# Kernel tuning notes

Measured on AMD Instinct MI355X. Metric: run time of the kernel, lower is better.

## Reference

```python
import jax, jax.numpy as jnp
import numpy as np

H, D, J, T, IN = 8, 32, 22, 6, 256   # heads, head_dim, joint_num, time_len-2, input_dim
S = 3 * J                            # sequence axis of attention (66)
NEG = -9e15


def _domain_mask():
    m = np.ones((S, S), np.float32)
    m[0:J, 2 * J:3 * J] = 0.0
    m[2 * J:3 * J, 0:J] = 0.0
    return jnp.asarray(m)


def setup_inputs() -> dict:
    key = jax.random.key(0)
    ks = jax.random.split(key, 5)
    s = 0.02
    return {
        "x": jax.random.normal(ks[0], (512, T, S, IN), jnp.float32),
        "Wq": jax.random.normal(ks[1], (H * D, IN), jnp.float32) * s,
        "bq": jnp.zeros((H * D,), jnp.float32),
        "Wk": jax.random.normal(ks[2], (H * D, IN), jnp.float32) * s,
        "bk": jnp.zeros((H * D,), jnp.float32),
        "Wv": jax.random.normal(ks[3], (H * D, IN), jnp.float32) * s,
        "bv": jnp.zeros((H * D,), jnp.float32),
        "Wc": jax.random.normal(ks[4], (J, S), jnp.float32) * s,
        "bc": jnp.zeros((J,), jnp.float32),
    }


def reference(x, Wq, bq, Wk, bk, Wv, bv, Wc, bc):
    B = x.shape[0]
    mask = _domain_mask()

    def proj(W, b):
        # (B,T,S,IN) @ (IN,H*D) -> (B,T,S,H,D) -> (B,T,H,S,D)
        return (x @ W.T + b).reshape(B, T, S, H, D).transpose(0, 1, 3, 2, 4)

    q = proj(Wq, bq)
    k = proj(Wk, bk)
    v = jax.nn.relu(proj(Wv, bv))

    scores = jnp.einsum('bthqd,bthkd->bthqk', q, k) / jnp.sqrt(jnp.float32(D))
    scores = scores * mask
    # joint_num == 22 branch: threshold-based pruning against row max
    m = jnp.max(scores, axis=-1, keepdims=True)
    scores = jnp.where(jnp.abs(scores) <= m / 9.0, NEG, scores)
    attn = jax.nn.softmax(scores, axis=-1)

    out = jnp.einsum('bthqk,bthkd->bthqd', attn, v)          # (B,T,H,S,D)
    # cls Linear over the S axis: (B,T,H,D,S) -> (B,T,H,D,J), then back to (B,T,H,J,D)
    out = jnp.einsum('bthsd,js->bthjd', out, Wc) + bc[None, None, None, :, None]
    out = out.transpose(0, 1, 3, 2, 4)                        # (B,T,J,H,D)
    return out.reshape(B, T * J, H * D)
```

## Files before the change

### kernel.cpp

```cpp
#include <hip/hip_runtime.h>
#include <hip/hip_bf16.h>


constexpr int T  = 6;
constexpr int S  = 66;
constexpr int IN = 256;
constexpr int H  = 8;
constexpr int D  = 32;
constexpr int J  = 22;
constexpr float NEG = -9e15f;
constexpr float INV_SQRT_D = 0.17677669529663688110f;

#define XH_OFF   0
#define XL_OFF   9216
#define WH_OFF   18432
#define WL_OFF   30720
#define QH_OFF   0
#define QL_OFF   4752
#define KH_OFF   9504
#define KL_OFF   14256
#define SC_OFF   19008
#define VTH_OFF  36432
#define VTL_OFF  43088
#define INV_OFF  49744
#define PH_OFF   0
#define PL_OFF   13728
#define AOT_OFF  27456
#define WCH_OFF  36432
#define WCL_OFF  43088
#define SMEM_BYTES 50008

#define WSW_STRIDE 24576
#define WSWC_OFF   786432
#define WS_W       799744ull
#define XIMG_OFF   799744
#define XIMG_BT    73728
#define WS_FULL    (799744ull + 3072ull * 73728ull)

typedef float f32x4  __attribute__((ext_vector_type(4)));
typedef short bf16x8 __attribute__((ext_vector_type(8)));
typedef short s4v    __attribute__((ext_vector_type(4)));

__device__ __forceinline__ unsigned cvtpk(float a, float b) {
    unsigned r;
    asm("v_cvt_pk_bf16_f32 %0, %1, %2" : "=v"(r) : "v"(a), "v"(b));
    return r;
}
__device__ __forceinline__ float bfh2f(unsigned short h) {
    return __uint_as_float(((unsigned)h) << 16);
}
__device__ __forceinline__ void split2(float a, float b, unsigned& hi, unsigned& lo) {
    unsigned h = cvtpk(a, b);
    float ra = a - __uint_as_float(h << 16);
    float rb = b - __uint_as_float(h & 0xffff0000u);
    lo = cvtpk(ra, rb);
    hi = h;
}
__device__ __forceinline__ bf16x8 ld_bf16x8_a8(const short* p) {
    s4v a = *(const s4v*)p;
    s4v b = *(const s4v*)(p + 4);
    return __builtin_shufflevector(a, b, 0, 1, 2, 3, 4, 5, 6, 7);
}
__device__ __forceinline__ void gload16(const void* g, void* l) {
    __builtin_amdgcn_global_load_lds(
        (const __attribute__((address_space(1))) unsigned*)g,
        (__attribute__((address_space(3))) unsigned*)l, 16, 0, 0);
}

__global__ __launch_bounds__(256)
void presplit_kernel(const float* __restrict__ Wq, const float* __restrict__ Wk,
                     const float* __restrict__ Wv, const float* __restrict__ Wc,
                     unsigned char* __restrict__ ws)
{
    int gid = blockIdx.x * 256 + threadIdx.x;
    if (gid < 49152) {
        int c   = gid & 15;
        int r2  = gid >> 4;
        int row = r2 % 96;
        int r3  = r2 / 96;
        int mat = row >> 5, dd = row & 31;
        int chunk = r3 & 3, hh = r3 >> 2;
        const float* Wm = (mat == 0) ? Wq : (mat == 1) ? Wk : Wv;
        float4 v = *(const float4*)(Wm + (size_t)(hh * 32 + dd) * IN + chunk * 64 + c * 4);
        uint2 hi, lo;
        split2(v.x, v.y, hi.x, lo.x);
        split2(v.z, v.w, hi.y, lo.y);
        unsigned base = (unsigned)r3 * WSW_STRIDE;
        unsigned rel  = (unsigned)(((row << 7) + (c << 3)) ^ ((row & 7) << 4));
        *(uint2*)(ws + base + rel)         = hi;
        *(uint2*)(ws + base + 12288 + rel) = lo;
    } else if (gid < 49152 + 1664) {
        int g2  = gid - 49152;
        int row = g2 / 52, cu = g2 - row * 52;
        int c0  = 2 * cu;
        float a = (row < 22 && c0     < 66) ? Wc[row * 66 + c0]     : 0.f;
        float b = (row < 22 && c0 + 1 < 66) ? Wc[row * 66 + c0 + 1] : 0.f;
        unsigned hi, lo;
        split2(a, b, hi, lo);
        *(unsigned*)(ws + WSWC_OFF + row * 208 + 4 * cu)        = hi;
        *(unsigned*)(ws + WSWC_OFF + 6656 + row * 208 + 4 * cu) = lo;
    }
}

__global__ __launch_bounds__(256)
void presplit_x_kernel(const float* __restrict__ x, unsigned char* __restrict__ ws)
{
    int gid = blockIdx.x * 256 + threadIdx.x;
    if (gid >= 3072 * 66 * 64) return;
    int c16  = gid & 63;
    int rest = gid >> 6;
    int s  = rest % 66;
    int bt = rest / 66;
    int chunk = c16 >> 4, c = c16 & 15;
    float4 v = *(const float4*)(x + (size_t)(bt * 66 + s) * 256 + c16 * 4);
    uint2 hi, lo;
    split2(v.x, v.y, hi.x, lo.x);
    split2(v.z, v.w, hi.y, lo.y);
    unsigned rel = (unsigned)(((s << 7) + (c << 3)) ^ ((s & 7) << 4));
    unsigned char* img = ws + XIMG_OFF + (size_t)bt * XIMG_BT + chunk * 18432;
    *(uint2*)(img + rel)        = hi;
    *(uint2*)(img + 9216 + rel) = lo;
}

template<int MODE>
__global__ __launch_bounds__(256, 3)
void mha_fused_kernel(const float* __restrict__ x,
                      const float* __restrict__ Wq, const float* __restrict__ bq,
                      const float* __restrict__ Wk, const float* __restrict__ bk,
                      const float* __restrict__ Wv, const float* __restrict__ bv,
                      const float* __restrict__ Wc, const float* __restrict__ bc,
                      const unsigned char* __restrict__ ws,
                      float* __restrict__ out)
{
    __shared__ __align__(16) unsigned char smem[SMEM_BYTES];

    const int tid = threadIdx.x;
    const int i0  = blockIdx.x;
    const int h   = (i0 >> 3) & 7;
    const int bt  = (i0 & 7) | ((i0 >> 6) << 3);

    const int wid  = tid >> 6;
    const int lane = tid & 63;
    const int l15  = lane & 15;
    const int quad = lane >> 4;
    const int swz  = (l15 & 7) << 4;

    f32x4 accs[8];
    #pragma unroll
    for (int jj = 0; jj < 8; ++jj) accs[jj] = (f32x4){0.f, 0.f, 0.f, 0.f};

    for (int chunk = 0; chunk < 4; ++chunk) {
        __syncthreads();
        if constexpr (MODE == 2) {
            const unsigned char* ximg = ws + XIMG_OFF + (size_t)bt * XIMG_BT + chunk * 18432;
            const unsigned char* wimg = ws + (unsigned)((h << 2) | chunk) * WSW_STRIDE;
            for (int i = wid; i < 18; i += 4)
                gload16(ximg + (i << 10) + (lane << 4), smem + XH_OFF + (i << 10));
            for (int i = wid; i < 24; i += 4)
                gload16(wimg + (i << 10) + (lane << 4), smem + WH_OFF + (i << 10));
        } else {
            if constexpr (MODE == 1) {
                const unsigned char* wimg = ws + (unsigned)((h << 2) | chunk) * WSW_STRIDE;
                for (int i = wid; i < 24; i += 4)
                    gload16(wimg + (i << 10) + (lane << 4), smem + WH_OFF + (i << 10));
            } else {
                for (int u = tid; u < 1536; u += 256) {
                    int row = u >> 4, c = u & 15;
                    int mat = row >> 5, dd = row & 31;
                    const float* Wm = (mat == 0) ? Wq : (mat == 1) ? Wk : Wv;
                    float4 v = *(const float4*)(Wm + (size_t)(h * 32 + dd) * IN + chunk * 64 + c * 4);
                    uint2 hi, lo;
                    split2(v.x, v.y, hi.x, lo.x);
                    split2(v.z, v.w, hi.y, lo.y);
                    int rel = ((row << 7) + (c << 3)) ^ ((row & 7) << 4);
                    *(uint2*)(smem + WH_OFF + rel) = hi;
                    *(uint2*)(smem + WL_OFF + rel) = lo;
                }
            }
            const float* xg = x + (size_t)bt * S * IN + chunk * 64;
            for (int u = tid; u < 1056; u += 256) {
                int s = u >> 4, c = u & 15;
                float4 v = *(const float4*)(xg + (size_t)s * IN + c * 4);
                uint2 hi, lo;
                split2(v.x, v.y, hi.x, lo.x);
                split2(v.z, v.w, hi.y, lo.y);
                int rel = ((s << 7) + (c << 3)) ^ ((s & 7) << 4);
                *(uint2*)(smem + XH_OFF + rel) = hi;
                *(uint2*)(smem + XL_OFF + rel) = lo;
            }
        }
        __syncthreads();

        const unsigned char* sb = smem;
        for (int jj = 0; jj < 8; ++jj) {
            int j = wid + 4 * jj;
            if (j >= 30) break;
            int mat = j / 10, rr = j - mat * 10;
            int mtile = rr >> 1, ntile = rr & 1;
            int abase = XH_OFF + ((mtile * 16 + l15) << 7);
            int bbase = WH_OFF + (((mat << 5) + (ntile << 4) + l15) << 7);
            #pragma unroll
            for (int kk = 0; kk < 2; ++kk) {
                int off = ((quad << 4) + (kk << 6)) ^ swz;
                bf16x8 ah = *(const bf16x8*)(sb + abase + off);
                bf16x8 al = *(const bf16x8*)(sb + abase + 9216 + off);
                bf16x8 bh = *(const bf16x8*)(sb + bbase + off);
                bf16x8 bl = *(const bf16x8*)(sb + bbase + 12288 + off);
                accs[jj] = __builtin_amdgcn_mfma_f32_16x16x32_bf16(ah, bh, accs[jj], 0, 0, 0);
                accs[jj] = __builtin_amdgcn_mfma_f32_16x16x32_bf16(ah, bl, accs[jj], 0, 0, 0);
                accs[jj] = __builtin_amdgcn_mfma_f32_16x16x32_bf16(al, bh, accs[jj], 0, 0, 0);
            }
        }
    }
    __syncthreads();

    {
        short* qh = (short*)(smem + QH_OFF); short* ql = (short*)(smem + QL_OFF);
        short* kh = (short*)(smem + KH_OFF); short* kl = (short*)(smem + KL_OFF);
        for (int jj = 0; jj < 8; ++jj) {
            int j = wid + 4 * jj;
            if (j >= 30) break;
            int mat = j / 10, rr = j - mat * 10;
            int mtile = rr >> 1, ntile = rr & 1;
            int dd = ntile * 16 + l15;
            const float* bias_p = (mat == 0) ? bq : (mat == 1) ? bk : bv;
            float bias = bias_p[h * 32 + dd];
            int sbase = mtile * 16 + quad * 4;
            if (mat < 2) {
                short* bh_ = (mat == 0) ? qh : kh;
                short* bl_ = (mat == 0) ? ql : kl;
                uint2 hi, lo;
                split2(accs[jj][0] + bias, accs[jj][1] + bias, hi.x, lo.x);
                split2(accs[jj][2] + bias, accs[jj][3] + bias, hi.y, lo.y);
                unsigned hs[4] = { hi.x & 0xffffu, hi.x >> 16, hi.y & 0xffffu, hi.y >> 16 };
                unsigned ls[4] = { lo.x & 0xffffu, lo.x >> 16, lo.y & 0xffffu, lo.y >> 16 };
                #pragma unroll
                for (int reg = 0; reg < 4; ++reg) {
                    int s = sbase + reg;
                    if (s < 66) {
                        bh_[s * 36 + dd] = (short)hs[reg];
                        bl_[s * 36 + dd] = (short)ls[reg];
                    }
                }
            } else {
                float vv[4];
                #pragma unroll
                for (int reg = 0; reg < 4; ++reg) {
                    int s = sbase + reg;
                    vv[reg] = (s < 66) ? fmaxf(accs[jj][reg] + bias, 0.f) : 0.f;
                }
                uint2 ph, pl;
                split2(vv[0], vv[1], ph.x, pl.x);
                split2(vv[2], vv[3], ph.y, pl.y);
                *(uint2*)(smem + VTH_OFF + dd * 208 + 2 * sbase) = ph;
                *(uint2*)(smem + VTL_OFF + dd * 208 + 2 * sbase) = pl;
            }
        }
        for (int u = tid; u < 512; u += 256) {
            int comp = u >= 256 ? 1 : 0, rem = comp ? u - 256 : u;
            int row = rem >> 3, kcol = 80 + 2 * (rem & 7);
            *(unsigned*)(smem + (comp ? VTL_OFF : VTH_OFF) + row * 208 + 2 * kcol) = 0u;
        }
    }
    __syncthreads();

    {
        const short* qh = (const short*)(smem + QH_OFF);
        const short* ql = (const short*)(smem + QL_OFF);
        const short* kh = (const short*)(smem + KH_OFF);
        const short* kl = (const short*)(smem + KL_OFF);
        float* sc = (float*)(smem + SC_OFF);
        for (int t = 0; t < 7; ++t) {
            int tt = wid + 4 * t;
            if (tt >= 25) break;
            int mq = tt / 5, mk = tt - mq * 5;
            int aoff = (mq * 16 + l15) * 36 + quad * 8;
            int boff = (mk * 16 + l15) * 36 + quad * 8;
            bf16x8 ah = ld_bf16x8_a8(qh + aoff);
            bf16x8 al = ld_bf16x8_a8(ql + aoff);
            bf16x8 bh = ld_bf16x8_a8(kh + boff);
            bf16x8 bl = ld_bf16x8_a8(kl + boff);
            f32x4 acc = (f32x4){0.f, 0.f, 0.f, 0.f};
            acc = __builtin_amdgcn_mfma_f32_16x16x32_bf16(ah, bh, acc, 0, 0, 0);
            acc = __builtin_amdgcn_mfma_f32_16x16x32_bf16(ah, bl, acc, 0, 0, 0);
            acc = __builtin_amdgcn_mfma_f32_16x16x32_bf16(al, bh, acc, 0, 0, 0);
            int ks = mk * 16 + l15;
            #pragma unroll
            for (int reg = 0; reg < 4; ++reg) {
                int qs = mq * 16 + quad * 4 + reg;
                if (qs < 66 && ks < 66) {
                    bool masked = (qs < J && ks >= 2 * J) || (qs >= 2 * J && ks < J);
                    sc[qs * 66 + ks] = masked ? 0.f : acc[reg] * INV_SQRT_D;
                }
            }
        }
    }
    __syncthreads();

    {
        const float* sc = (const float*)(smem + SC_OFF);
        const int group = tid >> 4, lane16 = tid & 15;
        const int rbase = ((group & 3) << 2) + (group >> 2);
        float val[5][5];
        #pragma unroll
        for (int i = 0; i < 5; ++i) {
            int r = rbase + 16 * i;
            #pragma unroll
            for (int tt = 0; tt < 5; ++tt) {
                int c = lane16 + 16 * tt;
                val[i][tt] = (r < 66 && c < 66) ? sc[r * 66 + c] : -INFINITY;
            }
        }
        __syncthreads();

        short* Ph = (short*)(smem + PH_OFF);
        short* Pl = (short*)(smem + PL_OFF);
        float* inv = (float*)(smem + INV_OFF);
        #pragma unroll
        for (int i = 0; i < 5; ++i) {
            int r = rbase + 16 * i;
            if (r >= 66) continue;
            float m = -INFINITY;
            #pragma unroll
            for (int tt = 0; tt < 5; ++tt) m = fmaxf(m, val[i][tt]);
            m = fmaxf(m, __shfl_xor(m, 1));
            m = fmaxf(m, __shfl_xor(m, 2));
            m = fmaxf(m, __shfl_xor(m, 4));
            m = fmaxf(m, __shfl_xor(m, 8));
            const float thr = m / 9.0f;
            float e[5], lsum = 0.f, rmax = -INFINITY;
            #pragma unroll
            for (int tt = 0; tt < 5; ++tt) {
                float sv = val[i][tt];
                float pr = (fabsf(sv) <= thr) ? NEG : sv;
                val[i][tt] = pr;
                rmax = fmaxf(rmax, pr);
            }
            rmax = fmaxf(rmax, __shfl_xor(rmax, 1));
            rmax = fmaxf(rmax, __shfl_xor(rmax, 2));
            rmax = fmaxf(rmax, __shfl_xor(rmax, 4));
            rmax = fmaxf(rmax, __shfl_xor(rmax, 8));
            #pragma unroll
            for (int tt = 0; tt < 5; ++tt) {
                int c = lane16 + 16 * tt;
                float ev = (c < 66) ? __expf(val[i][tt] - rmax) : 0.f;
                e[tt] = ev;
                lsum += ev;
            }
            lsum += __shfl_xor(lsum, 1);
            lsum += __shfl_xor(lsum, 2);
            lsum += __shfl_xor(lsum, 4);
            lsum += __shfl_xor(lsum, 8);
            #pragma unroll
            for (int tt = 0; tt < 6; ++tt) {
                int c = lane16 + 16 * tt;
                unsigned short hi = 0, lo = 0;
                if (c < 66) {
                    float ev = e[tt];
                    hi = (unsigned short)cvtpk(ev, ev);
                    lo = (unsigned short)cvtpk(ev - bfh2f(hi), 0.f);
                }
                if (c < 96) {
                    Ph[r * 104 + c] = (short)hi;
                    Pl[r * 104 + c] = (short)lo;
                }
            }
            if (lane16 == 0) inv[r] = 1.0f / lsum;
        }
    }
    __syncthreads();

    {
        const short* Ph = (const short*)(smem + PH_OFF);
        const short* Pl = (const short*)(smem + PL_OFF);
        const short* vh = (const short*)(smem + VTH_OFF);
        const short* vl = (const short*)(smem + VTL_OFF);
        const float* inv = (const float*)(smem + INV_OFF);
        for (int t = 0; t < 3; ++t) {
            int tt = wid + 4 * t;
            if (tt >= 10) break;
            int mq = tt >> 1, nd = tt & 1;
            f32x4 acc = (f32x4){0.f, 0.f, 0.f, 0.f};
            #pragma unroll
            for (int ks = 0; ks < 3; ++ks) {
                bf16x8 a   = *(const bf16x8*)(Ph + (mq * 16 + l15) * 104 + ks * 32 + quad * 8);
                bf16x8 al8 = *(const bf16x8*)(Pl + (mq * 16 + l15) * 104 + ks * 32 + quad * 8);
                bf16x8 b   = *(const bf16x8*)(vh + (nd * 16 + l15) * 104 + ks * 32 + quad * 8);
                bf16x8 bl8 = *(const bf16x8*)(vl + (nd * 16 + l15) * 104 + ks * 32 + quad * 8);
                acc = __builtin_amdgcn_mfma_f32_16x16x32_bf16(a, b, acc, 0, 0, 0);
                acc = __builtin_amdgcn_mfma_f32_16x16x32_bf16(al8, b, acc, 0, 0, 0);
                acc = __builtin_amdgcn_mfma_f32_16x16x32_bf16(a, bl8, acc, 0, 0, 0);
            }
            int dd = nd * 16 + l15, sbase = mq * 16 + quad * 4;
            float o[4];
            #pragma unroll
            for (int reg = 0; reg < 4; ++reg) {
                int qs = sbase + reg;
                o[reg] = (qs < 66) ? acc[reg] * inv[qs] : 0.f;
            }
            uint2 pk;
            pk.x = cvtpk(o[0], o[1]);
            pk.y = cvtpk(o[2], o[3]);
            *(uint2*)(smem + AOT_OFF + dd * 208 + 2 * sbase) = pk;
        }
        for (int u = tid; u < 384; u += 256) {
            int row = u / 12, kcol = 80 + 2 * (u % 12);
            *(unsigned*)(smem + AOT_OFF + row * 208 + 2 * kcol) = 0u;
        }
    }
    __syncthreads();

    if constexpr (MODE >= 1) {
        const unsigned char* wc = ws + WSWC_OFF;
        for (int i = wid; i < 13; i += 4)
            gload16(wc + (i << 10) + (lane << 4), smem + WCH_OFF + (i << 10));
    } else {
        for (int u = tid; u < 726; u += 256) {
            int row = u / 33, cp = u - row * 33;
            float2 w = *(const float2*)(Wc + row * 66 + 2 * cp);
            unsigned hi, lo;
            split2(w.x, w.y, hi, lo);
            *(unsigned*)(smem + WCH_OFF + row * 208 + 4 * cp) = hi;
            *(unsigned*)(smem + WCL_OFF + row * 208 + 4 * cp) = lo;
        }
        for (int u = tid; u < 836; u += 256) {
            int comp = u >= 418 ? 1 : 0, rem = comp ? u - 418 : u;
            int row = rem / 19, kcol = 66 + 2 * (rem % 19);
            *(unsigned*)(smem + (comp ? WCL_OFF : WCH_OFF) + row * 208 + 2 * kcol) = 0u;
        }
    }
    __syncthreads();

    {
        const short* Wch = (const short*)(smem + WCH_OFF);
        const short* Wcl = (const short*)(smem + WCL_OFF);
        const short* aoT = (const short*)(smem + AOT_OFF);
        int mj = wid >> 1, nd = wid & 1;
        f32x4 acc = (f32x4){0.f, 0.f, 0.f, 0.f};
        #pragma unroll
        for (int ks = 0; ks < 3; ++ks) {
            bf16x8 a   = *(const bf16x8*)(Wch + (mj * 16 + l15) * 104 + ks * 32 + quad * 8);
            bf16x8 al8 = *(const bf16x8*)(Wcl + (mj * 16 + l15) * 104 + ks * 32 + quad * 8);
            bf16x8 b   = *(const bf16x8*)(aoT + (nd * 16 + l15) * 104 + ks * 32 + quad * 8);
            acc = __builtin_amdgcn_mfma_f32_16x16x32_bf16(a, b, acc, 0, 0, 0);
            acc = __builtin_amdgcn_mfma_f32_16x16x32_bf16(al8, b, acc, 0, 0, 0);
        }
        int dd = nd * 16 + l15;
        #pragma unroll
        for (int reg = 0; reg < 4; ++reg) {
            int j = mj * 16 + quad * 4 + reg;
            if (j < 22) {
                size_t o = (size_t)(bt * J + j) * (H * D) + h * 32 + dd;
                out[o] = acc[reg] + bc[j];
            }
        }
    }
}

extern "C" void kernel_launch(void* const* d_in, const int* in_sizes, int n_in,
                              void* d_out, int out_size, void* d_ws, size_t ws_size,
                              hipStream_t stream) {
    const float* x  = (const float*)d_in[0];
    const float* Wq = (const float*)d_in[1];
    const float* bq = (const float*)d_in[2];
    const float* Wk = (const float*)d_in[3];
    const float* bk = (const float*)d_in[4];
    const float* Wv = (const float*)d_in[5];
    const float* bv = (const float*)d_in[6];
    const float* Wc = (const float*)d_in[7];
    const float* bc = (const float*)d_in[8];
    float* out = (float*)d_out;

    const int B = 512;
    dim3 grid(B * T * H), block(256);
    if (d_ws != nullptr && ws_size >= WS_FULL) {
        hipLaunchKernelGGL(presplit_kernel, dim3(199), dim3(256), 0, stream,
                           Wq, Wk, Wv, Wc, (unsigned char*)d_ws);
        hipLaunchKernelGGL(presplit_x_kernel, dim3(50688), dim3(256), 0, stream,
                           x, (unsigned char*)d_ws);
        hipLaunchKernelGGL((mha_fused_kernel<2>), grid, block, 0, stream,
                           x, Wq, bq, Wk, bk, Wv, bv, Wc, bc,
                           (const unsigned char*)d_ws, out);
    } else if (d_ws != nullptr && ws_size >= WS_W) {
        hipLaunchKernelGGL(presplit_kernel, dim3(199), dim3(256), 0, stream,
                           Wq, Wk, Wv, Wc, (unsigned char*)d_ws);
        hipLaunchKernelGGL((mha_fused_kernel<1>), grid, block, 0, stream,
                           x, Wq, bq, Wk, bk, Wv, bv, Wc, bc,
                           (const unsigned char*)d_ws, out);
    } else {
        hipLaunchKernelGGL((mha_fused_kernel<0>), grid, block, 0, stream,
                           x, Wq, bq, Wk, bk, Wv, bv, Wc, bc,
                           (const unsigned char*)nullptr, out);
    }
}
```

Baseline: 974.0 us.

## Switch QKV projection to 32x32x16 MFMA with fragment-ordered pre-split images

Replaces the 16x16x32 bf16 MFMA tiling of the QKV projection with 32x32x16 MFMAs, giving 9 output tiles over 4 waves instead of 30 small tiles. The weight and x images in the workspace are re-laid out in MFMA fragment order, so each lane loads its operand with one contiguous 16-byte read and needs no swizzle. The x pre-split kernel now goes through LDS to build the padded 96-row image, which enlarges the x workspace. The goal is fewer MFMA issues and fewer LDS address computations, at the cost of padding waste (96 rows for 66) and uneven work across waves (three waves get 2 tiles, one gets 3). The V-tail zeroing loop was removed; the padded rows now come out as zeros from the relu branch for s>=66, but columns 96..103 may no longer be cleared.

```diff
diff --git a/kernel.cpp b/kernel.cpp
--- a/kernel.cpp
+++ b/kernel.cpp
@@ -12,9 +12,8 @@
 constexpr float INV_SQRT_D = 0.17677669529663688110f;
 
 #define XH_OFF   0
-#define XL_OFF   9216
-#define WH_OFF   18432
-#define WL_OFF   30720
+#define WH_OFF   24576
+#define FRAG_LO  12288
 #define QH_OFF   0
 #define QL_OFF   4752
 #define KH_OFF   9504
@@ -34,12 +33,13 @@
 #define WSWC_OFF   786432
 #define WS_W       799744ull
 #define XIMG_OFF   799744
-#define XIMG_BT    73728
-#define WS_FULL    (799744ull + 3072ull * 73728ull)
-
-typedef float f32x4  __attribute__((ext_vector_type(4)));
-typedef short bf16x8 __attribute__((ext_vector_type(8)));
-typedef short s4v    __attribute__((ext_vector_type(4)));
+#define XIMG_BT    98304
+#define WS_FULL    (799744ull + 3072ull * 98304ull)
+
+typedef float f32x4   __attribute__((ext_vector_type(4)));
+typedef float f32x16  __attribute__((ext_vector_type(16)));
+typedef short bf16x8  __attribute__((ext_vector_type(8)));
+typedef short s4v     __attribute__((ext_vector_type(4)));
 
 __device__ __forceinline__ unsigned cvtpk(float a, float b) {
     unsigned r;
@@ -74,21 +74,21 @@
 {
     int gid = blockIdx.x * 256 + threadIdx.x;
     if (gid < 49152) {
-        int c   = gid & 15;
-        int r2  = gid >> 4;
-        int row = r2 % 96;
-        int r3  = r2 / 96;
+        int img = gid / 1536, u = gid - img * 1536;
+        int row = u >> 4, c = u & 15, k0 = c << 2;
         int mat = row >> 5, dd = row & 31;
-        int chunk = r3 & 3, hh = r3 >> 2;
+        int chunk = img & 3, hh = img >> 2;
         const float* Wm = (mat == 0) ? Wq : (mat == 1) ? Wk : Wv;
         float4 v = *(const float4*)(Wm + (size_t)(hh * 32 + dd) * IN + chunk * 64 + c * 4);
         uint2 hi, lo;
         split2(v.x, v.y, hi.x, lo.x);
         split2(v.z, v.w, hi.y, lo.y);
-        unsigned base = (unsigned)r3 * WSW_STRIDE;
-        unsigned rel  = (unsigned)(((row << 7) + (c << 3)) ^ ((row & 7) << 4));
-        *(uint2*)(ws + base + rel)         = hi;
-        *(uint2*)(ws + base + 12288 + rel) = lo;
+        int tile  = (mat << 2) + (k0 >> 4);
+        int lanei = dd + (((k0 >> 3) & 1) << 5);
+        int byte  = (tile << 10) + (lanei << 4) + ((k0 & 7) << 1);
+        unsigned char* base = ws + (size_t)img * WSW_STRIDE;
+        *(uint2*)(base + byte)           = hi;
+        *(uint2*)(base + FRAG_LO + byte) = lo;
     } else if (gid < 49152 + 1664) {
         int g2  = gid - 49152;
         int row = g2 / 52, cu = g2 - row * 52;
@@ -105,21 +105,35 @@
 __global__ __launch_bounds__(256)
 void presplit_x_kernel(const float* __restrict__ x, unsigned char* __restrict__ ws)
 {
-    int gid = blockIdx.x * 256 + threadIdx.x;
-    if (gid >= 3072 * 66 * 64) return;
-    int c16  = gid & 63;
-    int rest = gid >> 6;
-    int s  = rest % 66;
-    int bt = rest / 66;
-    int chunk = c16 >> 4, c = c16 & 15;
-    float4 v = *(const float4*)(x + (size_t)(bt * 66 + s) * 256 + c16 * 4);
-    uint2 hi, lo;
-    split2(v.x, v.y, hi.x, lo.x);
-    split2(v.z, v.w, hi.y, lo.y);
-    unsigned rel = (unsigned)(((s << 7) + (c << 3)) ^ ((s & 7) << 4));
-    unsigned char* img = ws + XIMG_OFF + (size_t)bt * XIMG_BT + chunk * 18432;
-    *(uint2*)(img + rel)        = hi;
-    *(uint2*)(img + 9216 + rel) = lo;
+    __shared__ __align__(16) unsigned char lds[24576];
+    const int tid = threadIdx.x;
+    const int chunk = blockIdx.x & 3;
+    const int bt = blockIdx.x >> 2;
+    const float* xg = x + (size_t)bt * S * IN + chunk * 64;
+    for (int u = tid; u < 1536; u += 256) {
+        int s = u >> 4, c = u & 15;
+        int rel = ((s << 7) + (c << 3)) ^ ((s & 7) << 4);
+        uint2 hi = {0u, 0u}, lo = {0u, 0u};
+        if (s < 66) {
+            float4 v = *(const float4*)(xg + (size_t)s * IN + c * 4);
+            split2(v.x, v.y, hi.x, lo.x);
+            split2(v.z, v.w, hi.y, lo.y);
+        }
+        *(uint2*)(lds + rel)         = hi;
+        *(uint2*)(lds + 12288 + rel) = lo;
+    }
+    __syncthreads();
+    const int lane = tid & 63, wid = tid >> 6;
+    unsigned char* img = ws + XIMG_OFF + (size_t)bt * XIMG_BT + chunk * 24576;
+    for (int i = wid; i < 24; i += 4) {
+        int comp = (i >= 12) ? 1 : 0;
+        int ti = i - comp * 12;
+        int mtile = ti >> 2, ks = ti & 3;
+        int row = mtile * 32 + (lane & 31);
+        int rel = ((row << 7) + (ks << 5) + ((lane >> 5) << 4)) ^ ((row & 7) << 4);
+        uint4 v = *(const uint4*)(lds + comp * 12288 + rel);
+        *(uint4*)(img + (i << 10) + (lane << 4)) = v;
+    }
 }
 
 template<int MODE>
@@ -143,72 +157,74 @@
     const int lane = tid & 63;
     const int l15  = lane & 15;
     const int quad = lane >> 4;
-    const int swz  = (l15 & 7) << 4;
-
-    f32x4 accs[8];
-    #pragma unroll
-    for (int jj = 0; jj < 8; ++jj) accs[jj] = (f32x4){0.f, 0.f, 0.f, 0.f};
+
+    const f32x16 zacc = {0.f,0.f,0.f,0.f,0.f,0.f,0.f,0.f,0.f,0.f,0.f,0.f,0.f,0.f,0.f,0.f};
+    f32x16 accs[3] = {zacc, zacc, zacc};
 
     for (int chunk = 0; chunk < 4; ++chunk) {
         __syncthreads();
         if constexpr (MODE == 2) {
-            const unsigned char* ximg = ws + XIMG_OFF + (size_t)bt * XIMG_BT + chunk * 18432;
-            const unsigned char* wimg = ws + (unsigned)((h << 2) | chunk) * WSW_STRIDE;
-            for (int i = wid; i < 18; i += 4)
+            const unsigned char* ximg = ws + XIMG_OFF + (size_t)bt * XIMG_BT + chunk * 24576;
+            const unsigned char* wimg = ws + (size_t)((h << 2) | chunk) * WSW_STRIDE;
+            for (int i = wid; i < 24; i += 4)
                 gload16(ximg + (i << 10) + (lane << 4), smem + XH_OFF + (i << 10));
             for (int i = wid; i < 24; i += 4)
                 gload16(wimg + (i << 10) + (lane << 4), smem + WH_OFF + (i << 10));
         } else {
             if constexpr (MODE == 1) {
-                const unsigned char* wimg = ws + (unsigned)((h << 2) | chunk) * WSW_STRIDE;
+                const unsigned char* wimg = ws + (size_t)((h << 2) | chunk) * WSW_STRIDE;
                 for (int i = wid; i < 24; i += 4)
                     gload16(wimg + (i << 10) + (lane << 4), smem + WH_OFF + (i << 10));
             } else {
                 for (int u = tid; u < 1536; u += 256) {
-                    int row = u >> 4, c = u & 15;
-                    int mat = row >> 5, dd = row & 31;
+                    int row = u >> 4, c = u & 15, k0 = c << 2;
+                    int mat = row >> 5, dd2 = row & 31;
                     const float* Wm = (mat == 0) ? Wq : (mat == 1) ? Wk : Wv;
-                    float4 v = *(const float4*)(Wm + (size_t)(h * 32 + dd) * IN + chunk * 64 + c * 4);
+                    float4 v = *(const float4*)(Wm + (size_t)(h * 32 + dd2) * IN + chunk * 64 + c * 4);
                     uint2 hi, lo;
                     split2(v.x, v.y, hi.x, lo.x);
                     split2(v.z, v.w, hi.y, lo.y);
-                    int rel = ((row << 7) + (c << 3)) ^ ((row & 7) << 4);
-                    *(uint2*)(smem + WH_OFF + rel) = hi;
-                    *(uint2*)(smem + WL_OFF + rel) = lo;
+                    int tile  = (mat << 2) + (k0 >> 4);
+                    int lanei = dd2 + (((k0 >> 3) & 1) << 5);
+                    int byte  = (tile << 10) + (lanei << 4) + ((k0 & 7) << 1);
+                    *(uint2*)(smem + WH_OFF + byte)           = hi;
+                    *(uint2*)(smem + WH_OFF + FRAG_LO + byte) = lo;
                 }
             }
             const float* xg = x + (size_t)bt * S * IN + chunk * 64;
-            for (int u = tid; u < 1056; u += 256) {
-                int s = u >> 4, c = u & 15;
-                float4 v = *(const float4*)(xg + (size_t)s * IN + c * 4);
-                uint2 hi, lo;
-                split2(v.x, v.y, hi.x, lo.x);
-                split2(v.z, v.w, hi.y, lo.y);
-                int rel = ((s << 7) + (c << 3)) ^ ((s & 7) << 4);
-                *(uint2*)(smem + XH_OFF + rel) = hi;
-                *(uint2*)(smem + XL_OFF + rel) = lo;
+            for (int u = tid; u < 1536; u += 256) {
+                int s = u >> 4, c = u & 15, k0 = c << 2;
+                uint2 hi = {0u, 0u}, lo = {0u, 0u};
+                if (s < 66) {
+                    float4 v = *(const float4*)(xg + (size_t)s * IN + c * 4);
+                    split2(v.x, v.y, hi.x, lo.x);
+                    split2(v.z, v.w, hi.y, lo.y);
+                }
+                int tile  = ((s >> 5) << 2) + (k0 >> 4);
+                int lanei = (s & 31) + (((k0 >> 3) & 1) << 5);
+                int byte  = (tile << 10) + (lanei << 4) + ((k0 & 7) << 1);
+                *(uint2*)(smem + XH_OFF + byte)           = hi;
+                *(uint2*)(smem + XH_OFF + FRAG_LO + byte) = lo;
             }
         }
         __syncthreads();
 
-        const unsigned char* sb = smem;
-        for (int jj = 0; jj < 8; ++jj) {
-            int j = wid + 4 * jj;
-            if (j >= 30) break;
-            int mat = j / 10, rr = j - mat * 10;
-            int mtile = rr >> 1, ntile = rr & 1;
-            int abase = XH_OFF + ((mtile * 16 + l15) << 7);
-            int bbase = WH_OFF + (((mat << 5) + (ntile << 4) + l15) << 7);
-            #pragma unroll
-            for (int kk = 0; kk < 2; ++kk) {
-                int off = ((quad << 4) + (kk << 6)) ^ swz;
-                bf16x8 ah = *(const bf16x8*)(sb + abase + off);
-                bf16x8 al = *(const bf16x8*)(sb + abase + 9216 + off);
-                bf16x8 bh = *(const bf16x8*)(sb + bbase + off);
-                bf16x8 bl = *(const bf16x8*)(sb + bbase + 12288 + off);
-                accs[jj] = __builtin_amdgcn_mfma_f32_16x16x32_bf16(ah, bh, accs[jj], 0, 0, 0);
-                accs[jj] = __builtin_amdgcn_mfma_f32_16x16x32_bf16(ah, bl, accs[jj], 0, 0, 0);
-                accs[jj] = __builtin_amdgcn_mfma_f32_16x16x32_bf16(al, bh, accs[jj], 0, 0, 0);
+        #pragma unroll
+        for (int t = 0; t < 3; ++t) {
+            int p = wid + 4 * t;
+            if (p >= 9) break;
+            int mtile = p / 3, mat = p - mtile * 3;
+            const unsigned char* xa = smem + XH_OFF + ((mtile * 4) << 10) + (lane << 4);
+            const unsigned char* wb = smem + WH_OFF + ((mat   * 4) << 10) + (lane << 4);
+            #pragma unroll
+            for (int ks = 0; ks < 4; ++ks) {
+                bf16x8 ah = *(const bf16x8*)(xa + (ks << 10));
+                bf16x8 al = *(const bf16x8*)(xa + (ks << 10) + FRAG_LO);
+                bf16x8 bh = *(const bf16x8*)(wb + (ks << 10));
+                bf16x8 bl = *(const bf16x8*)(wb + (ks << 10) + FRAG_LO);
+                accs[t] = __builtin_amdgcn_mfma_f32_32x32x16_bf16(ah, bh, accs[t], 0, 0, 0);
+                accs[t] = __builtin_amdgcn_mfma_f32_32x32x16_bf16(ah, bl, accs[t], 0, 0, 0);
+                accs[t] = __builtin_amdgcn_mfma_f32_32x32x16_bf16(al, bh, accs[t], 0, 0, 0);
             }
         }
     }
@@ -217,49 +233,52 @@
     {
         short* qh = (short*)(smem + QH_OFF); short* ql = (short*)(smem + QL_OFF);
         short* kh = (short*)(smem + KH_OFF); short* kl = (short*)(smem + KL_OFF);
-        for (int jj = 0; jj < 8; ++jj) {
-            int j = wid + 4 * jj;
-            if (j >= 30) break;
-            int mat = j / 10, rr = j - mat * 10;
-            int mtile = rr >> 1, ntile = rr & 1;
-            int dd = ntile * 16 + l15;
+        const int dd = lane & 31;
+        const int half = lane >> 5;
+        #pragma unroll
+        for (int t = 0; t < 3; ++t) {
+            int p = wid + 4 * t;
+            if (p >= 9) break;
+            int mtile = p / 3, mat = p - mtile * 3;
             const float* bias_p = (mat == 0) ? bq : (mat == 1) ? bk : bv;
             float bias = bias_p[h * 32 + dd];
-            int sbase = mtile * 16 + quad * 4;
             if (mat < 2) {
                 short* bh_ = (mat == 0) ? qh : kh;
                 short* bl_ = (mat == 0) ? ql : kl;
-                uint2 hi, lo;
-                split2(accs[jj][0] + bias, accs[jj][1] + bias, hi.x, lo.x);
-                split2(accs[jj][2] + bias, accs[jj][3] + bias, hi.y, lo.y);
-                unsigned hs[4] = { hi.x & 0xffffu, hi.x >> 16, hi.y & 0xffffu, hi.y >> 16 };
-                unsigned ls[4] = { lo.x & 0xffffu, lo.x >> 16, lo.y & 0xffffu, lo.y >> 16 };
                 #pragma unroll
-                for (int reg = 0; reg < 4; ++reg) {
-                    int s = sbase + reg;
-                    if (s < 66) {
-                        bh_[s * 36 + dd] = (short)hs[reg];
-                        bl_[s * 36 + dd] = (short)ls[reg];
+                for (int g = 0; g < 4; ++g) {
+                    int sb2 = mtile * 32 + half * 4 + 8 * g;
+                    uint2 hi, lo;
+                    split2(accs[t][4*g+0] + bias, accs[t][4*g+1] + bias, hi.x, lo.x);
+                    split2(accs[t][4*g+2] + bias, accs[t][4*g+3] + bias, hi.y, lo.y);
+                    unsigned hs[4] = { hi.x & 0xffffu, hi.x >> 16, hi.y & 0xffffu, hi.y >> 16 };
+                    unsigned ls[4] = { lo.x & 0xffffu, lo.x >> 16, lo.y & 0xffffu, lo.y >> 16 };
+                    #pragma unroll
+                    for (int r = 0; r < 4; ++r) {
+                        int s = sb2 + r;
+                        if (s < 66) {
+                            bh_[s * 36 + dd] = (short)hs[r];
+                            bl_[s * 36 + dd] = (short)ls[r];
+                        }
                     }
                 }
             } else {
-                float vv[4];
                 #pragma unroll
-                for (int reg = 0; reg < 4; ++reg) {
-                    int s = sbase + reg;
-                    vv[reg] = (s < 66) ? fmaxf(accs[jj][reg] + bias, 0.f) : 0.f;
-                }
-                uint2 ph, pl;
-                split2(vv[0], vv[1], ph.x, pl.x);
-                split2(vv[2], vv[3], ph.y, pl.y);
-                *(uint2*)(smem + VTH_OFF + dd * 208 + 2 * sbase) = ph;
-                *(uint2*)(smem + VTL_OFF + dd * 208 + 2 * sbase) = pl;
-            }
-        }
-        for (int u = tid; u < 512; u += 256) {
-            int comp = u >= 256 ? 1 : 0, rem = comp ? u - 256 : u;
-            int row = rem >> 3, kcol = 80 + 2 * (rem & 7);
-            *(unsigned*)(smem + (comp ? VTL_OFF : VTH_OFF) + row * 208 + 2 * kcol) = 0u;
+                for (int g = 0; g < 4; ++g) {
+                    int sb2 = mtile * 32 + half * 4 + 8 * g;
+                    float vv[4];
+                    #pragma unroll
+                    for (int r = 0; r < 4; ++r) {
+                        int s = sb2 + r;
+                        vv[r] = (s < 66) ? fmaxf(accs[t][4*g+r] + bias, 0.f) : 0.f;
+                    }
+                    uint2 ph, pl;
+                    split2(vv[0], vv[1], ph.x, pl.x);
+                    split2(vv[2], vv[3], ph.y, pl.y);
+                    *(uint2*)(smem + VTH_OFF + dd * 208 + 2 * sb2) = ph;
+                    *(uint2*)(smem + VTL_OFF + dd * 208 + 2 * sb2) = pl;
+                }
+            }
         }
     }
     __syncthreads();
@@ -476,7 +495,7 @@
     if (d_ws != nullptr && ws_size >= WS_FULL) {
         hipLaunchKernelGGL(presplit_kernel, dim3(199), dim3(256), 0, stream,
                            Wq, Wk, Wv, Wc, (unsigned char*)d_ws);
-        hipLaunchKernelGGL(presplit_x_kernel, dim3(50688), dim3(256), 0, stream,
+        hipLaunchKernelGGL(presplit_x_kernel, dim3(12288), dim3(256), 0, stream,
                            x, (unsigned char*)d_ws);
         hipLaunchKernelGGL((mha_fused_kernel<2>), grid, block, 0, stream,
                            x, Wq, bq, Wk, bk, Wv, bv, Wc, bc,
```

Result: slower. 1.015 ms (+4.2%).
